# Kernel tuning notes

Measured on AMD Instinct MI355X. Metric: run time of the kernel, lower is better.

## Reference

```python
import jax, jax.numpy as jnp
import numpy as np

DIM = 768
DEPTH = 12
HEADS = 12
DIM_HEAD = DIM // HEADS
DIM_MLP = 3072
PATCH = 16
SPECTRA = 4096
NUM_PATCHES = SPECTRA // PATCH
NUM_CLASSES = 1000
SCALE = DIM_HEAD ** -0.5
EPS = 1e-5


def sincos_pos_embed(embed_dim, n_pos):
    omega = np.arange(embed_dim // 2, dtype=np.float64) / (embed_dim / 2.0)
    omega = 1.0 / 10000 ** omega
    pos = np.arange(n_pos, dtype=np.float64)
    out = np.einsum('m,d->md', pos, omega)
    emb = np.concatenate([np.sin(out), np.cos(out)], axis=1)
    emb = np.concatenate([np.zeros([1, embed_dim]), emb], axis=0)  # cls slot
    return jnp.asarray(emb, jnp.float32)  # [N+1, D]


def setup_inputs() -> dict:
    key = jax.random.key(0)
    ks = jax.random.split(key, 12)
    s = 0.02
    d = {
        'x': jax.random.normal(ks[0], (32, 1, SPECTRA), jnp.float32),
        'conv_w': jax.random.normal(ks[1], (PATCH, DIM), jnp.float32) * s,
        'conv_b': jnp.zeros((DIM,), jnp.float32),
        'pos_embed': sincos_pos_embed(DIM, NUM_PATCHES),
        'cls_token': jax.random.normal(ks[2], (1, DIM), jnp.float32) * s,
        'ln1_w': jnp.ones((DEPTH, DIM), jnp.float32),
        'ln1_b': jnp.zeros((DEPTH, DIM), jnp.float32),
        'qkv_w': jax.random.normal(ks[3], (DEPTH, DIM, 3 * DIM), jnp.float32) * s,
        'out_w': jax.random.normal(ks[4], (DEPTH, DIM, DIM), jnp.float32) * s,
        'out_b': jnp.zeros((DEPTH, DIM), jnp.float32),
        'ln2_w': jnp.ones((DEPTH, DIM), jnp.float32),
        'ln2_b': jnp.zeros((DEPTH, DIM), jnp.float32),
        'mlp_w1': jax.random.normal(ks[5], (DEPTH, DIM, DIM_MLP), jnp.float32) * s,
        'mlp_b1': jnp.zeros((DEPTH, DIM_MLP), jnp.float32),
        'mlp_w2': jax.random.normal(ks[6], (DEPTH, DIM_MLP, DIM), jnp.float32) * s,
        'mlp_b2': jnp.zeros((DEPTH, DIM), jnp.float32),
        'cls_ln_w': jnp.ones((DIM,), jnp.float32),
        'cls_ln_b': jnp.zeros((DIM,), jnp.float32),
        'head_w': jax.random.normal(ks[7], (DIM, NUM_CLASSES), jnp.float32) * s,
        'head_b': jnp.zeros((NUM_CLASSES,), jnp.float32),
    }
    return d


def _ln(z, w, b):
    mu = z.mean(-1, keepdims=True)
    var = ((z - mu) ** 2).mean(-1, keepdims=True)
    return (z - mu) / jnp.sqrt(var + EPS) * w + b


def _forward(x, conv_w, conv_b, pos_embed, cls_token,
             ln1_w, ln1_b, qkv_w, out_w, out_b, ln2_w, ln2_b,
             mlp_w1, mlp_b1, mlp_w2, mlp_b2,
             cls_ln_w, cls_ln_b, head_w, head_b):
    B = x.shape[0]
    # Conv1d(1, D, k=P, stride=P) == non-overlapping patch linear proj
    patches = x.reshape(B, NUM_PATCHES, PATCH)
    h = patches @ conv_w + conv_b                         # [B, N, D]
    h = h + pos_embed[1:]
    cls = cls_token + pos_embed[:1]                       # [1, D]
    h = jnp.concatenate([jnp.broadcast_to(cls[None], (B, 1, DIM)), h], axis=1)  # [B, N+1, D]

    def block(h, p):
        l1w, l1b, qw, ow, ob, l2w, l2b, w1, b1, w2, b2 = p
        skip = h
        z = _ln(h, l1w, l1b)
        qkv = z @ qw                                      # [B, n, 3D]
        q, k, v = jnp.split(qkv, 3, axis=-1)
        def heads(t):
            return t.reshape(B, -1, HEADS, DIM_HEAD).transpose(0, 2, 1, 3)
        q, k, v = heads(q), heads(k), heads(v)            # [B, H, n, dh]
        dots = jnp.einsum('bhid,bhjd->bhij', q, k) * SCALE
        attn = jax.nn.softmax(dots, axis=-1)
        o = jnp.einsum('bhij,bhjd->bhid', attn, v)
        o = o.transpose(0, 2, 1, 3).reshape(B, -1, DIM)
        h = o @ ow + ob + skip
        skip = h
        z = _ln(h, l2w, l2b)
        z = jax.nn.gelu(z @ w1 + b1, approximate=False) @ w2 + b2
        return z + skip, None

    params = (ln1_w, ln1_b, qkv_w, out_w, out_b, ln2_w, ln2_b,
              mlp_w1, mlp_b1, mlp_w2, mlp_b2)
    h, _ = jax.lax.scan(block, h, params)
    cls_out = _ln(h[:, 0], cls_ln_w, cls_ln_b)
    return cls_out @ head_w + head_b                      # [B, num_classes]


def reference(x, conv_w, conv_b, pos_embed, cls_token,
              ln1_w, ln1_b, qkv_w, out_w, out_b, ln2_w, ln2_b,
              mlp_w1, mlp_b1, mlp_w2, mlp_b2,
              cls_ln_w, cls_ln_b, head_w, head_b):
    return _forward(x, conv_w, conv_b, pos_embed, cls_token,
                    ln1_w, ln1_b, qkv_w, out_w, out_b, ln2_w, ln2_b,
                    mlp_w1, mlp_b1, mlp_w2, mlp_b2,
                    cls_ln_w, cls_ln_b, head_w, head_b)
```

## Files before the change

kernel.cpp:

```cpp
#include <hip/hip_runtime.h>
#include <math.h>

#define DIM 768
#define DEPTH 12
#define HEADS 12
#define DIM_HEAD 64
#define DIM_MLP 3072
#define PATCH 16
#define NUM_PATCHES 256
#define SEQ 257
#define NUM_CLASSES 1000
#define BATCH 32
#define SCALE 0.125f
#define EPS 1e-5f
#define ROWS 8224
#define PAD_ROWS 8320
#define PAD_A 8448

#define WL_QKV 0
#define WL_OW  (2304 * 768)
#define WL_W1  (WL_OW + 768 * 768)
#define WL_W2  (WL_W1 + 3072 * 768)
#define WL_TOT (WL_W2 + 768 * 3072)

typedef short bf16x8 __attribute__((ext_vector_type(8)));
typedef float f32x4 __attribute__((ext_vector_type(4)));

__device__ inline unsigned short f2bf(float f) {
    union { float f; unsigned int u; } c; c.f = f;
    unsigned int u = c.u;
    return (unsigned short)((u + 0x7fffu + ((u >> 16) & 1u)) >> 16);
}

#define MFMA16(d, a, b) d = __builtin_amdgcn_mfma_f32_16x16x32_bf16(a, b, d, 0, 0, 0)
#define SBAR() asm volatile("s_barrier" ::: "memory")
#define LGKM0() asm volatile("s_waitcnt lgkmcnt(0)" ::: "memory")

__global__ void patch_embed_kernel(const float* __restrict__ x,
                                   const float* __restrict__ conv_w,
                                   const float* __restrict__ conv_b,
                                   const float* __restrict__ pos,
                                   const float* __restrict__ cls_tok,
                                   float* __restrict__ h) {
    int row = blockIdx.x;
    int b = row / SEQ;
    int r = row % SEQ;
    int t = threadIdx.x;
    float* out = h + (long)row * DIM;
    if (r == 0) {
        for (int d = t; d < DIM; d += 256)
            out[d] = cls_tok[d] + pos[d];
        return;
    }
    int p = r - 1;
    const float* xp = x + (long)b * 4096 + p * PATCH;
    float xv[PATCH];
#pragma unroll
    for (int k = 0; k < PATCH; ++k) xv[k] = xp[k];
    for (int d = t; d < DIM; d += 256) {
        float acc = conv_b[d];
#pragma unroll
        for (int k = 0; k < PATCH; ++k)
            acc += xv[k] * conv_w[k * DIM + d];
        out[d] = acc + pos[(long)r * DIM + d];
    }
}

template <int OBF>
__global__ __launch_bounds__(256) void layernorm2_kernel(
    const float* __restrict__ in, long in_stride,
    const float* __restrict__ w, const float* __restrict__ bia,
    void* __restrict__ out) {
    long row = (long)blockIdx.x * 4 + (threadIdx.x >> 6);
    int lane = threadIdx.x & 63;
    const float4* src = (const float4*)(in + row * in_stride);
    float4 v[3];
#pragma unroll
    for (int k = 0; k < 3; ++k) v[k] = src[lane + 64 * k];
    float s = 0.f, q = 0.f;
#pragma unroll
    for (int k = 0; k < 3; ++k) {
        s += v[k].x + v[k].y + v[k].z + v[k].w;
        q += v[k].x * v[k].x + v[k].y * v[k].y + v[k].z * v[k].z + v[k].w * v[k].w;
    }
#pragma unroll
    for (int off = 1; off < 64; off <<= 1) {
        s += __shfl_xor(s, off);
        q += __shfl_xor(q, off);
    }
    float mu = s * (1.0f / DIM);
    float rstd = rsqrtf(q * (1.0f / DIM) - mu * mu + EPS);
    const float4* w4 = (const float4*)w;
    const float4* b4 = (const float4*)bia;
#pragma unroll
    for (int k = 0; k < 3; ++k) {
        float4 wv = w4[lane + 64 * k], bv = b4[lane + 64 * k];
        float o0 = (v[k].x - mu) * rstd * wv.x + bv.x;
        float o1 = (v[k].y - mu) * rstd * wv.y + bv.y;
        float o2 = (v[k].z - mu) * rstd * wv.z + bv.z;
        float o3 = (v[k].w - mu) * rstd * wv.w + bv.w;
        if (OBF) {
            ushort4 pv;
            pv.x = f2bf(o0); pv.y = f2bf(o1); pv.z = f2bf(o2); pv.w = f2bf(o3);
            ((ushort4*)((unsigned short*)out + row * DIM))[lane + 64 * k] = pv;
        } else {
            float4 ov = make_float4(o0, o1, o2, o3);
            ((float4*)((float*)out + row * DIM))[lane + 64 * k] = ov;
        }
    }
}

template <int LAYERS>
__global__ __launch_bounds__(256) void transpose_all_kernel(
    const float* __restrict__ qw, const float* __restrict__ ow,
    const float* __restrict__ w1, const float* __restrict__ w2,
    unsigned short* __restrict__ wOut) {
    __shared__ float tile[64][68];
    int t = blockIdx.x;
    int l = t / 1728; t -= l * 1728;
    const float* src; unsigned short* dst; int K, N, kt, nt;
    unsigned short* wL = wOut + (long)l * WL_TOT;
    if (t < 432)       {            src = qw + (long)l * 768 * 2304; dst = wL + WL_QKV; K = 768;  N = 2304; kt = t % 12; nt = t / 12; }
    else if (t < 576)  { t -= 432;  src = ow + (long)l * 768 * 768;  dst = wL + WL_OW;  K = 768;  N = 768;  kt = t % 12; nt = t / 12; }
    else if (t < 1152) { t -= 576;  src = w1 + (long)l * 768 * 3072; dst = wL + WL_W1;  K = 768;  N = 3072; kt = t % 12; nt = t / 12; }
    else               { t -= 1152; src = w2 + (long)l * 3072 * 768; dst = wL + WL_W2;  K = 3072; N = 768;  kt = t % 48; nt = t / 48; }
    int k0 = kt * 64, n0 = nt * 64;
    int tid = threadIdx.x;
    {
        int r0 = tid >> 4, c4 = (tid & 15) * 4;
#pragma unroll
        for (int p = 0; p < 4; ++p) {
            int r = r0 + p * 16;
            float4 v = *(const float4*)(src + (long)(k0 + r) * N + n0 + c4);
            tile[r][c4 + 0] = v.x; tile[r][c4 + 1] = v.y;
            tile[r][c4 + 2] = v.z; tile[r][c4 + 3] = v.w;
        }
    }
    __syncthreads();
    {
        int nr0 = tid >> 3, kc8 = (tid & 7) * 8;
#pragma unroll
        for (int p = 0; p < 2; ++p) {
            int nr = nr0 + p * 32;
            short vv[8];
#pragma unroll
            for (int e = 0; e < 8; ++e)
                vv[e] = (short)f2bf(tile[kc8 + e][nr]);
            *(bf16x8*)(dst + (long)(n0 + nr) * K + k0 + kc8) = *(bf16x8*)vv;
        }
    }
}

__global__ __launch_bounds__(512) void attn2_kernel(const unsigned short* __restrict__ qkv,
                                                    unsigned short* __restrict__ o) {
    __shared__ unsigned short sh[75264];
    const int tid = threadIdx.x;
    const int lane = tid & 63;
    const int w = tid >> 6;

    const int nwg = gridDim.x;
    const int orig = blockIdx.x;
    const int q = nwg >> 3, r = nwg & 7;
    const int xcd = orig & 7, idx = orig >> 3;
    const int wg = (xcd < r ? xcd * (q + 1) : r * (q + 1) + (xcd - r) * q) + idx;
    const int bh = wg / 3, qc = wg % 3;
    const int b = bh / HEADS, hh = bh % HEADS;
    const unsigned short* qbase = qkv + (long)b * SEQ * 2304 + hh * 64;
    const unsigned short* kbase = qbase + 768;
    const unsigned short* vbase = qbase + 1536;

#pragma unroll
    for (int u = 0; u < 5; ++u) {
        int c = tid + u * 512;
        if (c < 2304) {
            int j = c >> 3, cb = c & 7;
            int gj = j > 256 ? 256 : j;
            const unsigned short* g = kbase + (long)gj * 2304 + ((cb ^ (j & 7)) << 3);
            __builtin_amdgcn_global_load_lds(
                (const __attribute__((address_space(1))) void*)g,
                (__attribute__((address_space(3))) void*)&sh[j * 64 + cb * 8], 16, 0, 0);
        }
    }
#pragma unroll
    for (int u = 0; u < 5; ++u) {
        int c = tid + u * 512;
        if (c < 2304) {
            int j = c >> 3, dc = c & 7;
            short vv[8] = {0, 0, 0, 0, 0, 0, 0, 0};
            if (j < SEQ) *(bf16x8*)vv = *(const bf16x8*)(vbase + (long)j * 2304 + dc * 8);
#pragma unroll
            for (int e = 0; e < 8; ++e)
                sh[18432 + (dc * 8 + e) * 296 + j] = (unsigned short)vv[e];
        }
    }
    __syncthreads();

    const int arow = qc * 128 + w * 16 + (lane & 15);
    const int garow = arow > 256 ? 256 : arow;
    f32x4 s[18] = {};
#pragma unroll
    for (int ks = 0; ks < 2; ++ks) {
        bf16x8 aq = *(const bf16x8*)(qbase + (long)garow * 2304 + ks * 32 + (lane >> 4) * 8);
        int cb = ks * 4 + (lane >> 4);
#pragma unroll
        for (int nf = 0; nf < 18; ++nf) {
            int brow = nf * 16 + (lane & 15);
            bf16x8 bk = *(const bf16x8*)&sh[brow * 64 + ((cb ^ (brow & 7)) << 3)];
            MFMA16(s[nf], aq, bk);
        }
    }

    float inv[4];
#pragma unroll
    for (int j = 0; j < 4; ++j) {
        float m_ = -3.0e38f;
#pragma unroll
        for (int nf = 0; nf < 18; ++nf) {
            int col = nf * 16 + (lane & 15);
            float xv = (col < SEQ) ? s[nf][j] * SCALE : -3.0e38f;
            s[nf][j] = xv;
            m_ = fmaxf(m_, xv);
        }
#pragma unroll
        for (int off = 1; off < 16; off <<= 1) m_ = fmaxf(m_, __shfl_xor(m_, off));
        float sm = 0.f;
#pragma unroll
        for (int nf = 0; nf < 18; ++nf) {
            float e = __expf(s[nf][j] - m_);
            s[nf][j] = e;
            sm += e;
        }
#pragma unroll
        for (int off = 1; off < 16; off <<= 1) sm += __shfl_xor(sm, off);
        inv[j] = 1.0f / sm;
    }
#pragma unroll
    for (int nf = 0; nf < 18; ++nf) {
        int col = nf * 16 + (lane & 15);
#pragma unroll
        for (int j = 0; j < 4; ++j) {
            int row = w * 16 + (lane >> 4) * 4 + j;
            sh[37376 + row * 296 + col] = f2bf(s[nf][j] * inv[j]);
        }
    }
    __syncthreads();

    f32x4 oa[4] = {};
    const int prow = w * 16 + (lane & 15);
#pragma unroll
    for (int ks = 0; ks < 9; ++ks) {
        bf16x8 ap = *(const bf16x8*)&sh[37376 + prow * 296 + ks * 32 + (lane >> 4) * 8];
#pragma unroll
        for (int n = 0; n < 4; ++n) {
            int drow = n * 16 + (lane & 15);
            bf16x8 bv = *(const bf16x8*)&sh[18432 + drow * 296 + ks * 32 + (lane >> 4) * 8];
            MFMA16(oa[n], ap, bv);
        }
    }
#pragma unroll
    for (int n = 0; n < 4; ++n) {
        int col = hh * 64 + n * 16 + (lane & 15);
#pragma unroll
        for (int j = 0; j < 4; ++j) {
            int gr = qc * 128 + w * 16 + (lane >> 4) * 4 + j;
            if (gr < SEQ)
                o[((long)(b * SEQ + gr)) * DIM + col] = f2bf(oa[n][j]);
        }
    }
}

template <int NK, int ACT, int OBF>
__global__ __launch_bounds__(256, 2) void gemmd_kernel(
    const unsigned short* __restrict__ A,
    const unsigned short* __restrict__ Bt,
    const float* __restrict__ bias,
    const float* __restrict__ resid,
    void* __restrict__ C,
    int M, int GY, int lda, int ldb, int ldc) {
    __shared__ unsigned short sh[32768];
    const int tid = threadIdx.x;
    const int lane = tid & 63;
    const int w = tid >> 6;
    const int wr = w >> 1, wc = w & 1;

    const int nwg = gridDim.x;
    const int orig = blockIdx.x;
    const int q = nwg >> 3, r = nwg & 7;
    const int xcd = orig & 7, idx = orig >> 3;
    const int wg = (xcd < r ? xcd * (q + 1) : r * (q + 1) + (xcd - r) * q) + idx;
    const int bm = (wg / GY) * 128;
    const int bn = (wg % GY) * 128;

    const unsigned short* Ag = A + (long)bm * lda;
    const unsigned short* Bg = Bt + (long)bn * ldb;

    auto stage = [&](int kt) {
        unsigned short* La = &sh[(kt & 1) * 16384];
        unsigned short* Lb = La + 8192;
#pragma unroll
        for (int u = 0; u < 4; ++u) {
            int c = tid + u * 256;
            int lr = c >> 3, cb = c & 7;
            int sw = (cb ^ (lr & 7)) << 3;
            const unsigned short* ga = Ag + (long)lr * lda + kt * 64 + sw;
            __builtin_amdgcn_global_load_lds(
                (const __attribute__((address_space(1))) void*)ga,
                (__attribute__((address_space(3))) void*)&La[lr * 64 + (cb << 3)], 16, 0, 0);
            const unsigned short* gb = Bg + (long)lr * ldb + kt * 64 + sw;
            __builtin_amdgcn_global_load_lds(
                (const __attribute__((address_space(1))) void*)gb,
                (__attribute__((address_space(3))) void*)&Lb[lr * 64 + (cb << 3)], 16, 0, 0);
        }
    };
    auto ldA = [&](int p, int m, int ks) {
        int row = wr * 64 + m * 16 + (lane & 15);
        int cb = ks * 4 + (lane >> 4);
        return *(const bf16x8*)&sh[p * 16384 + row * 64 + ((cb ^ (row & 7)) << 3)];
    };
    auto ldB = [&](int p, int n, int ks) {
        int row = wc * 64 + n * 16 + (lane & 15);
        int cb = ks * 4 + (lane >> 4);
        return *(const bf16x8*)&sh[p * 16384 + 8192 + row * 64 + ((cb ^ (row & 7)) << 3)];
    };

    f32x4 acc[4][4] = {};

    stage(0); stage(1);
    asm volatile("s_waitcnt vmcnt(8)" ::: "memory");
    SBAR();

    for (int kt = 0; kt < NK; ++kt) {
        const int p = kt & 1;
        bf16x8 a[4][2], b[4][2];
#pragma unroll
        for (int m = 0; m < 4; ++m) { a[m][0] = ldA(p, m, 0); a[m][1] = ldA(p, m, 1); }
#pragma unroll
        for (int n = 0; n < 4; ++n) { b[n][0] = ldB(p, n, 0); b[n][1] = ldB(p, n, 1); }
        SBAR();
        if (kt + 2 < NK) stage(kt + 2);
        LGKM0();
        __builtin_amdgcn_s_setprio(1);
#pragma unroll
        for (int m = 0; m < 4; ++m)
#pragma unroll
            for (int n = 0; n < 4; ++n) {
                MFMA16(acc[m][n], a[m][0], b[n][0]);
                MFMA16(acc[m][n], a[m][1], b[n][1]);
            }
        __builtin_amdgcn_s_setprio(0);
        if (kt + 2 < NK) {
            asm volatile("s_waitcnt vmcnt(8)" ::: "memory");
        } else if (kt + 1 < NK) {
            asm volatile("s_waitcnt vmcnt(0)" ::: "memory");
        }
        SBAR();
    }

#pragma unroll
    for (int mi = 0; mi < 4; ++mi) {
        int gr0 = bm + wr * 64 + mi * 16 + (lane >> 4) * 4;
#pragma unroll
        for (int ni = 0; ni < 4; ++ni) {
            int gc = bn + wc * 64 + ni * 16 + (lane & 15);
            float bv = bias ? bias[gc] : 0.f;
#pragma unroll
            for (int j = 0; j < 4; ++j) {
                int gr = gr0 + j;
                if (gr >= M) continue;
                float v = acc[mi][ni][j] + bv;
                if (ACT) v = 0.5f * v * (1.0f + erff(v * 0.70710678118654752f));
                long ci = (long)gr * ldc + gc;
                if (OBF) {
                    ((unsigned short*)C)[ci] = f2bf(v);
                } else {
                    if (resid) v += resid[ci];
                    ((float*)C)[ci] = v;
                }
            }
        }
    }
}

__global__ void gemm_f32_kernel(const float* __restrict__ A,
                                const float* __restrict__ W,
                                const float* __restrict__ bias,
                                float* __restrict__ C,
                                int M, int N, int K) {
    __shared__ float As[16][65];
    __shared__ float Bs[16][65];
    int bm = blockIdx.x * 64, bn = blockIdx.y * 64;
    int t = threadIdx.x;
    int tx = t & 15, ty = t >> 4;
    float acc[4][4] = {};
    for (int k0 = 0; k0 < K; k0 += 16) {
        {
            int ar = bm + (t >> 2);
            int ac = k0 + (t & 3) * 4;
            float4 av = make_float4(0.f, 0.f, 0.f, 0.f);
            if (ar < M) av = *(const float4*)(A + (long)ar * K + ac);
            int kk = (t & 3) * 4, rr = t >> 2;
            As[kk + 0][rr] = av.x; As[kk + 1][rr] = av.y;
            As[kk + 2][rr] = av.z; As[kk + 3][rr] = av.w;
        }
        {
            int wr2 = k0 + (t >> 4);
            int wc2 = bn + (t & 15) * 4;
            float4 wv;
            wv.x = (wc2 + 0 < N) ? W[(long)wr2 * N + wc2 + 0] : 0.f;
            wv.y = (wc2 + 1 < N) ? W[(long)wr2 * N + wc2 + 1] : 0.f;
            wv.z = (wc2 + 2 < N) ? W[(long)wr2 * N + wc2 + 2] : 0.f;
            wv.w = (wc2 + 3 < N) ? W[(long)wr2 * N + wc2 + 3] : 0.f;
            int kr = t >> 4, nc = (t & 15) * 4;
            Bs[kr][nc + 0] = wv.x; Bs[kr][nc + 1] = wv.y;
            Bs[kr][nc + 2] = wv.z; Bs[kr][nc + 3] = wv.w;
        }
        __syncthreads();
#pragma unroll
        for (int kk = 0; kk < 16; ++kk) {
            float a0 = As[kk][ty * 4 + 0], a1 = As[kk][ty * 4 + 1];
            float a2 = As[kk][ty * 4 + 2], a3 = As[kk][ty * 4 + 3];
            float b0 = Bs[kk][tx], b1 = Bs[kk][tx + 16];
            float b2 = Bs[kk][tx + 32], b3 = Bs[kk][tx + 48];
            acc[0][0] += a0 * b0; acc[0][1] += a0 * b1; acc[0][2] += a0 * b2; acc[0][3] += a0 * b3;
            acc[1][0] += a1 * b0; acc[1][1] += a1 * b1; acc[1][2] += a1 * b2; acc[1][3] += a1 * b3;
            acc[2][0] += a2 * b0; acc[2][1] += a2 * b1; acc[2][2] += a2 * b2; acc[2][3] += a2 * b3;
            acc[3][0] += a3 * b0; acc[3][1] += a3 * b1; acc[3][2] += a3 * b2; acc[3][3] += a3 * b3;
        }
        __syncthreads();
    }
#pragma unroll
    for (int i = 0; i < 4; ++i) {
        int r = bm + ty * 4 + i;
        if (r >= M) continue;
#pragma unroll
        for (int j = 0; j < 4; ++j) {
            int c = bn + tx + 16 * j;
            if (c >= N) continue;
            C[(long)r * N + c] = acc[i][j] + (bias ? bias[c] : 0.f);
        }
    }
}

extern "C" void kernel_launch(void* const* d_in, const int* in_sizes, int n_in,
                              void* d_out, int out_size, void* d_ws, size_t ws_size,
                              hipStream_t stream) {
    const float* x        = (const float*)d_in[0];
    const float* conv_w   = (const float*)d_in[1];
    const float* conv_b   = (const float*)d_in[2];
    const float* pos      = (const float*)d_in[3];
    const float* cls_tok  = (const float*)d_in[4];
    const float* ln1_w    = (const float*)d_in[5];
    const float* ln1_b    = (const float*)d_in[6];
    const float* qkv_w    = (const float*)d_in[7];
    const float* out_w    = (const float*)d_in[8];
    const float* out_b    = (const float*)d_in[9];
    const float* ln2_w    = (const float*)d_in[10];
    const float* ln2_b    = (const float*)d_in[11];
    const float* mlp_w1   = (const float*)d_in[12];
    const float* mlp_b1   = (const float*)d_in[13];
    const float* mlp_w2   = (const float*)d_in[14];
    const float* mlp_b2   = (const float*)d_in[15];
    const float* cls_ln_w = (const float*)d_in[16];
    const float* cls_ln_b = (const float*)d_in[17];
    const float* head_w   = (const float*)d_in[18];
    const float* head_b   = (const float*)d_in[19];
    float* out = (float*)d_out;

    char* cur = (char*)d_ws;
    auto alloc = [&](size_t bytes) {
        void* p = cur; cur += (bytes + 255) & ~(size_t)255; return p;
    };
    float*          h      = (float*)alloc((size_t)PAD_ROWS * DIM * 4);
    unsigned short* z_bf   = (unsigned short*)alloc((size_t)PAD_A * DIM * 2);
    unsigned short* qkv_bf = (unsigned short*)alloc((size_t)ROWS * 3 * DIM * 2);
    unsigned short* o_bf   = (unsigned short*)alloc((size_t)PAD_ROWS * DIM * 2);
    unsigned short* m1     = (unsigned short*)alloc((size_t)PAD_ROWS * DIM_MLP * 2);
    float*          clsz   = (float*)alloc((size_t)BATCH * DIM * 4);
    size_t used = (size_t)(cur - (char*)d_ws);
    bool all_layers = (ws_size - used) >= (size_t)12 * WL_TOT * 2 + 256;
    unsigned short* wAll = (unsigned short*)alloc((all_layers ? (size_t)12 : (size_t)1) * WL_TOT * 2);

    patch_embed_kernel<<<ROWS, 256, 0, stream>>>(x, conv_w, conv_b, pos, cls_tok, h);

    if (all_layers)
        transpose_all_kernel<12><<<12 * 1728, 256, 0, stream>>>(
            qkv_w, out_w, mlp_w1, mlp_w2, wAll);

    for (int l = 0; l < DEPTH; ++l) {
        unsigned short* wL = wAll + (all_layers ? (long)l * WL_TOT : 0);
        if (!all_layers)
            transpose_all_kernel<1><<<1728, 256, 0, stream>>>(
                qkv_w + (long)l * DIM * 3 * DIM, out_w + (long)l * DIM * DIM,
                mlp_w1 + (long)l * DIM * DIM_MLP, mlp_w2 + (long)l * DIM_MLP * DIM, wL);
        unsigned short* qkvwT = wL + WL_QKV;
        unsigned short* owT   = wL + WL_OW;
        unsigned short* w1T   = wL + WL_W1;
        unsigned short* w2T   = wL + WL_W2;

        layernorm2_kernel<1><<<ROWS / 4, 256, 0, stream>>>(
            h, DIM, ln1_w + (long)l * DIM, ln1_b + (long)l * DIM, z_bf);

        gemmd_kernel<12, 0, 1><<<65 * 18, 256, 0, stream>>>(
            z_bf, qkvwT, nullptr, nullptr, qkv_bf, ROWS, 18, DIM, DIM, 3 * DIM);

        attn2_kernel<<<384 * 3, 512, 0, stream>>>(qkv_bf, o_bf);

        gemmd_kernel<12, 0, 0><<<65 * 6, 256, 0, stream>>>(
            o_bf, owT, out_b + (long)l * DIM, h, h, ROWS, 6, DIM, DIM, DIM);

        layernorm2_kernel<1><<<ROWS / 4, 256, 0, stream>>>(
            h, DIM, ln2_w + (long)l * DIM, ln2_b + (long)l * DIM, z_bf);

        gemmd_kernel<12, 1, 1><<<65 * 24, 256, 0, stream>>>(
            z_bf, w1T, mlp_b1 + (long)l * DIM_MLP, nullptr, m1, ROWS, 24, DIM, DIM, DIM_MLP);

        gemmd_kernel<48, 0, 0><<<65 * 6, 256, 0, stream>>>(
            m1, w2T, mlp_b2 + (long)l * DIM, h, h, ROWS, 6, DIM_MLP, DIM_MLP, DIM);
    }

    layernorm2_kernel<0><<<BATCH / 4, 256, 0, stream>>>(
        h, (long)SEQ * DIM, cls_ln_w, cls_ln_b, clsz);
    gemm_f32_kernel<<<dim3(1, 16), 256, 0, stream>>>(
        clsz, head_w, head_b, out, BATCH, NUM_CLASSES, DIM);
}
```

Baseline: 4.132 ms.

## Pre-transpose V per head and add BK=32 GEMM variant for MLP up-projection

Adds a v_repack2 kernel that writes V transposed and padded per (batch, head), so attention can load it into LDS with async global_load_lds instead of scattered per-element LDS writes done three times per head. Adds a gemmd32 kernel with a 32-wide K step, smaller LDS footprint and 4 blocks per CU, and uses it for the W1 GEMM with GELU. Also pads the weight-transpose tile from 68 to 69 columns to reduce LDS bank conflicts. The cost is an extra launch and a round trip through global memory for V, plus half the K depth per pipeline stage in the new GEMM.

```diff
diff --git a/kernel.cpp b/kernel.cpp
--- a/kernel.cpp
+++ b/kernel.cpp
@@ -17,6 +17,9 @@
 #define PAD_ROWS 8320
 #define PAD_A 8448
 
+#define VT_LD 296
+#define VT_Z  (64 * VT_LD)
+
 #define WL_QKV 0
 #define WL_OW  (2304 * 768)
 #define WL_W1  (WL_OW + 768 * 768)
@@ -115,7 +118,7 @@
     const float* __restrict__ qw, const float* __restrict__ ow,
     const float* __restrict__ w1, const float* __restrict__ w2,
     unsigned short* __restrict__ wOut) {
-    __shared__ float tile[64][68];
+    __shared__ float tile[64][69];
     int t = blockIdx.x;
     int l = t / 1728; t -= l * 1728;
     const float* src; unsigned short* dst; int K, N, kt, nt;
@@ -151,7 +154,36 @@
     }
 }
 
+__global__ __launch_bounds__(256) void v_repack2_kernel(
+    const unsigned short* __restrict__ qkv, unsigned short* __restrict__ vt) {
+    __shared__ unsigned short lds[257 * 69 + 3];
+    int z = blockIdx.x;
+    int b = z / HEADS, hh = z % HEADS;
+    const unsigned short* vbase = qkv + (long)b * SEQ * 2304 + 1536 + hh * 64;
+    int tid = threadIdx.x;
+    for (int u = tid; u < 257 * 8; u += 256) {
+        int j = u >> 3, dc = u & 7;
+        bf16x8 v8 = *(const bf16x8*)(vbase + (long)j * 2304 + dc * 8);
+#pragma unroll
+        for (int e = 0; e < 8; ++e)
+            lds[j * 69 + dc * 8 + e] = (unsigned short)v8[e];
+    }
+    __syncthreads();
+    unsigned short* out = vt + (long)z * VT_Z;
+    for (int w = tid; w < 64 * 37; w += 256) {
+        int d = w / 37, jc = w % 37;
+        short vv[8];
+#pragma unroll
+        for (int e = 0; e < 8; ++e) {
+            int j = jc * 8 + e;
+            vv[e] = (j < SEQ) ? (short)lds[j * 69 + d] : (short)0;
+        }
+        *(bf16x8*)(out + d * VT_LD + jc * 8) = *(bf16x8*)vv;
+    }
+}
+
 __global__ __launch_bounds__(512) void attn2_kernel(const unsigned short* __restrict__ qkv,
+                                                    const unsigned short* __restrict__ vt,
                                                     unsigned short* __restrict__ o) {
     __shared__ unsigned short sh[75264];
     const int tid = threadIdx.x;
@@ -167,7 +199,6 @@
     const int b = bh / HEADS, hh = bh % HEADS;
     const unsigned short* qbase = qkv + (long)b * SEQ * 2304 + hh * 64;
     const unsigned short* kbase = qbase + 768;
-    const unsigned short* vbase = qbase + 1536;
 
 #pragma unroll
     for (int u = 0; u < 5; ++u) {
@@ -184,13 +215,11 @@
 #pragma unroll
     for (int u = 0; u < 5; ++u) {
         int c = tid + u * 512;
-        if (c < 2304) {
-            int j = c >> 3, dc = c & 7;
-            short vv[8] = {0, 0, 0, 0, 0, 0, 0, 0};
-            if (j < SEQ) *(bf16x8*)vv = *(const bf16x8*)(vbase + (long)j * 2304 + dc * 8);
-#pragma unroll
-            for (int e = 0; e < 8; ++e)
-                sh[18432 + (dc * 8 + e) * 296 + j] = (unsigned short)vv[e];
+        if (c < 2368) {
+            const unsigned short* g = vt + (long)bh * VT_Z + c * 8;
+            __builtin_amdgcn_global_load_lds(
+                (const __attribute__((address_space(1))) void*)g,
+                (__attribute__((address_space(3))) void*)&sh[18432 + c * 8], 16, 0, 0);
         }
     }
     __syncthreads();
@@ -253,7 +282,7 @@
 #pragma unroll
         for (int n = 0; n < 4; ++n) {
             int drow = n * 16 + (lane & 15);
-            bf16x8 bv = *(const bf16x8*)&sh[18432 + drow * 296 + ks * 32 + (lane >> 4) * 8];
+            bf16x8 bv = *(const bf16x8*)&sh[18432 + drow * VT_LD + ks * 32 + (lane >> 4) * 8];
             MFMA16(oa[n], ap, bv);
         }
     }
@@ -350,6 +379,116 @@
         __builtin_amdgcn_s_setprio(0);
         if (kt + 2 < NK) {
             asm volatile("s_waitcnt vmcnt(8)" ::: "memory");
+        } else if (kt + 1 < NK) {
+            asm volatile("s_waitcnt vmcnt(0)" ::: "memory");
+        }
+        SBAR();
+    }
+
+#pragma unroll
+    for (int mi = 0; mi < 4; ++mi) {
+        int gr0 = bm + wr * 64 + mi * 16 + (lane >> 4) * 4;
+#pragma unroll
+        for (int ni = 0; ni < 4; ++ni) {
+            int gc = bn + wc * 64 + ni * 16 + (lane & 15);
+            float bv = bias ? bias[gc] : 0.f;
+#pragma unroll
+            for (int j = 0; j < 4; ++j) {
+                int gr = gr0 + j;
+                if (gr >= M) continue;
+                float v = acc[mi][ni][j] + bv;
+                if (ACT) v = 0.5f * v * (1.0f + erff(v * 0.70710678118654752f));
+                long ci = (long)gr * ldc + gc;
+                if (OBF) {
+                    ((unsigned short*)C)[ci] = f2bf(v);
+                } else {
+                    if (resid) v += resid[ci];
+                    ((float*)C)[ci] = v;
+                }
+            }
+        }
+    }
+}
+
+template <int NK, int ACT, int OBF>
+__global__ __launch_bounds__(256, 4) void gemmd32_kernel(
+    const unsigned short* __restrict__ A,
+    const unsigned short* __restrict__ Bt,
+    const float* __restrict__ bias,
+    const float* __restrict__ resid,
+    void* __restrict__ C,
+    int M, int GY, int lda, int ldb, int ldc) {
+    __shared__ unsigned short sh[16384];
+    const int tid = threadIdx.x;
+    const int lane = tid & 63;
+    const int w = tid >> 6;
+    const int wr = w >> 1, wc = w & 1;
+
+    const int nwg = gridDim.x;
+    const int orig = blockIdx.x;
+    const int q = nwg >> 3, r = nwg & 7;
+    const int xcd = orig & 7, idx = orig >> 3;
+    const int wg = (xcd < r ? xcd * (q + 1) : r * (q + 1) + (xcd - r) * q) + idx;
+    const int bm = (wg / GY) * 128;
+    const int bn = (wg % GY) * 128;
+
+    const unsigned short* Ag = A + (long)bm * lda;
+    const unsigned short* Bg = Bt + (long)bn * ldb;
+
+    auto stage = [&](int kt) {
+        unsigned short* La = &sh[(kt & 1) * 8192];
+        unsigned short* Lb = La + 4096;
+#pragma unroll
+        for (int u = 0; u < 2; ++u) {
+            int c = tid + u * 256;
+            int lr = c >> 2, cb = c & 3;
+            int sw = (cb ^ (lr & 3)) << 3;
+            const unsigned short* ga = Ag + (long)lr * lda + kt * 32 + sw;
+            __builtin_amdgcn_global_load_lds(
+                (const __attribute__((address_space(1))) void*)ga,
+                (__attribute__((address_space(3))) void*)&La[lr * 32 + (cb << 3)], 16, 0, 0);
+            const unsigned short* gb = Bg + (long)lr * ldb + kt * 32 + sw;
+            __builtin_amdgcn_global_load_lds(
+                (const __attribute__((address_space(1))) void*)gb,
+                (__attribute__((address_space(3))) void*)&Lb[lr * 32 + (cb << 3)], 16, 0, 0);
+        }
+    };
+    auto ldA = [&](int p, int m) {
+        int row = wr * 64 + m * 16 + (lane & 15);
+        int cb = lane >> 4;
+        return *(const bf16x8*)&sh[p * 8192 + row * 32 + ((cb ^ (row & 3)) << 3)];
+    };
+    auto ldB = [&](int p, int n) {
+        int row = wc * 64 + n * 16 + (lane & 15);
+        int cb = lane >> 4;
+        return *(const bf16x8*)&sh[p * 8192 + 4096 + row * 32 + ((cb ^ (row & 3)) << 3)];
+    };
+
+    f32x4 acc[4][4] = {};
+
+    stage(0); stage(1);
+    asm volatile("s_waitcnt vmcnt(4)" ::: "memory");
+    SBAR();
+
+    for (int kt = 0; kt < NK; ++kt) {
+        const int p = kt & 1;
+        bf16x8 a[4], b[4];
+#pragma unroll
+        for (int m = 0; m < 4; ++m) a[m] = ldA(p, m);
+#pragma unroll
+        for (int n = 0; n < 4; ++n) b[n] = ldB(p, n);
+        SBAR();
+        if (kt + 2 < NK) stage(kt + 2);
+        LGKM0();
+        __builtin_amdgcn_s_setprio(1);
+#pragma unroll
+        for (int m = 0; m < 4; ++m)
+#pragma unroll
+            for (int n = 0; n < 4; ++n)
+                MFMA16(acc[m][n], a[m], b[n]);
+        __builtin_amdgcn_s_setprio(0);
+        if (kt + 2 < NK) {
+            asm volatile("s_waitcnt vmcnt(4)" ::: "memory");
         } else if (kt + 1 < NK) {
             asm volatile("s_waitcnt vmcnt(0)" ::: "memory");
         }
@@ -475,6 +614,7 @@
     unsigned short* qkv_bf = (unsigned short*)alloc((size_t)ROWS * 3 * DIM * 2);
     unsigned short* o_bf   = (unsigned short*)alloc((size_t)PAD_ROWS * DIM * 2);
     unsigned short* m1     = (unsigned short*)alloc((size_t)PAD_ROWS * DIM_MLP * 2);
+    unsigned short* vt     = (unsigned short*)alloc((size_t)BATCH * HEADS * VT_Z * 2);
     float*          clsz   = (float*)alloc((size_t)BATCH * DIM * 4);
     size_t used = (size_t)(cur - (char*)d_ws);
     bool all_layers = (ws_size - used) >= (size_t)12 * WL_TOT * 2 + 256;
@@ -503,7 +643,8 @@
         gemmd_kernel<12, 0, 1><<<65 * 18, 256, 0, stream>>>(
             z_bf, qkvwT, nullptr, nullptr, qkv_bf, ROWS, 18, DIM, DIM, 3 * DIM);
 
-        attn2_kernel<<<384 * 3, 512, 0, stream>>>(qkv_bf, o_bf);
+        v_repack2_kernel<<<BATCH * HEADS, 256, 0, stream>>>(qkv_bf, vt);
+        attn2_kernel<<<384 * 3, 512, 0, stream>>>(qkv_bf, vt, o_bf);
 
         gemmd_kernel<12, 0, 0><<<65 * 6, 256, 0, stream>>>(
             o_bf, owT, out_b + (long)l * DIM, h, h, ROWS, 6, DIM, DIM, DIM);
@@ -511,7 +652,7 @@
         layernorm2_kernel<1><<<ROWS / 4, 256, 0, stream>>>(
             h, DIM, ln2_w + (long)l * DIM, ln2_b + (long)l * DIM, z_bf);
 
-        gemmd_kernel<12, 1, 1><<<65 * 24, 256, 0, stream>>>(
+        gemmd32_kernel<24, 1, 1><<<65 * 24, 256, 0, stream>>>(
             z_bf, w1T, mlp_b1 + (long)l * DIM_MLP, nullptr, m1, ROWS, 24, DIM, DIM, DIM_MLP);
 
         gemmd_kernel<48, 0, 0><<<65 * 6, 256, 0, stream>>>(
```

Result: faster. 3.901 ms (-5.6%).
